# Kernel tuning notes

Measured on AMD Instinct MI355X. Metric: run time of the kernel, lower is better.

The kernel has to match this reference:

```python
import jax, jax.numpy as jnp
import numpy as np

N_NODES = 100000


def leaky(x):
    return jax.nn.leaky_relu(x, negative_slope=0.01)


def gcn_conv(h, W, b, src, dst, n_nodes):
    """PyG GCNConv: add self-loops, symmetric deg^{-1/2} normalization, scatter-add."""
    h = h @ W  # [N, out]
    deg = jax.ops.segment_sum(jnp.ones_like(dst, dtype=h.dtype), dst, num_segments=n_nodes) + 1.0  # +1 self-loop
    dinv = jax.lax.rsqrt(deg)  # deg >= 1 always
    norm = dinv[src] * dinv[dst]  # [E]
    msg = h[src] * norm[:, None]  # gather + scale, [E, out]
    agg = jax.ops.segment_sum(msg, dst, num_segments=n_nodes)
    agg = agg + h * (dinv * dinv)[:, None]  # self-loop message
    return agg + b


def setup_inputs() -> dict:
    key = jax.random.key(0)
    ks = jax.random.split(key, 16)
    num_teams = 100000
    n_edges = 5000000
    n_matches = 1000000
    x = jax.random.randint(ks[0], (N_NODES, 1), 0, num_teams)
    edge_index = jax.random.randint(ks[1], (2, n_edges), 0, N_NODES)
    home = jax.random.randint(ks[2], (n_matches,), 0, N_NODES)
    away = jax.random.randint(ks[3], (n_matches,), 0, N_NODES)
    emb = jax.random.normal(ks[4], (num_teams, 3), dtype=jnp.float32)
    W1 = jax.random.normal(ks[5], (3, 16), dtype=jnp.float32) * (1.0 / np.sqrt(3))
    b1 = jnp.zeros((16,), dtype=jnp.float32)
    W2 = jax.random.normal(ks[6], (16, 3), dtype=jnp.float32) * 0.25
    b2 = jnp.zeros((3,), dtype=jnp.float32)
    lw1 = jax.random.normal(ks[7], (6, 16), dtype=jnp.float32) * (1.0 / np.sqrt(6))
    lb1 = jnp.zeros((16,), dtype=jnp.float32)
    lw2 = jax.random.normal(ks[8], (16, 6), dtype=jnp.float32) * 0.25
    lb2 = jnp.zeros((6,), dtype=jnp.float32)
    lw3 = jax.random.normal(ks[9], (6, 3), dtype=jnp.float32) * (1.0 / np.sqrt(6))
    lb3 = jnp.zeros((3,), dtype=jnp.float32)
    return dict(x=x, edge_index=edge_index, home=home, away=away, emb=emb,
                W1=W1, b1=b1, W2=W2, b2=b2,
                lw1=lw1, lb1=lb1, lw2=lw2, lb2=lb2, lw3=lw3, lb3=lb3)


def reference(x, edge_index, home, away, emb, W1, b1, W2, b2, lw1, lb1, lw2, lb2, lw3, lb3):
    src, dst = edge_index[0], edge_index[1]
    h = emb[x[:, 0]]  # embedding lookup + squeeze(1) -> [N, 3]
    h = leaky(gcn_conv(h, W1, b1, src, dst, N_NODES))  # [N, 16]
    h = leaky(gcn_conv(h, W2, b2, src, dst, N_NODES))  # [N, 3]
    z = jnp.concatenate([h[home], h[away]], axis=-1)  # [M, 6]
    z = leaky(z @ lw1 + lb1)
    z = leaky(z @ lw2 + lb2)
    z = leaky(z @ lw3 + lb3)
    return z.reshape(-1, 3)
```

## Files before the change

### kernel.cpp

```cpp
#include <hip/hip_runtime.h>

typedef unsigned int u32;
typedef unsigned short u16;

static __device__ __forceinline__ float leaky(float v) {
    return v >= 0.0f ? v : 0.01f * v;
}

#define P1_CHUNK 8192
#define NBK 512
#define CAPB 16384
#define ASPLIT 4
#define S1F 8388608.0f
#define S2F 2097152.0f

__global__ __launch_bounds__(256) void k_p1scatterA(
        const int* __restrict__ src, const int* __restrict__ dst,
        int* __restrict__ cur, u32* __restrict__ bkt, int nE) {
    __shared__ int sc[NBK];
    __shared__ int loff[NBK];
    __shared__ int gb[NBK];
    __shared__ int lcur[NBK];
    __shared__ u32 pay[P1_CHUNK];
    __shared__ u16 bb[P1_CHUNK];
    int t = threadIdx.x;
    sc[t] = 0; sc[t + 256] = 0;
    __syncthreads();
    int base = blockIdx.x * P1_CHUNK;
    int lim = min(P1_CHUNK, nE - base);
    if (lim == P1_CHUNK) {
        const int4* p = (const int4*)(dst + base);
        for (int i = t; i < P1_CHUNK / 4; i += 256) {
            int4 v = p[i];
            atomicAdd(&sc[v.x >> 8], 1);
            atomicAdd(&sc[v.y >> 8], 1);
            atomicAdd(&sc[v.z >> 8], 1);
            atomicAdd(&sc[v.w >> 8], 1);
        }
    } else {
        for (int i = t; i < lim; i += 256)
            atomicAdd(&sc[dst[base + i] >> 8], 1);
    }
    __syncthreads();
    int c0 = sc[t], c1 = sc[t + 256];
    gb[t]       = (t << 14)         + ((c0 > 0) ? atomicAdd(&cur[t], c0) : 0);
    gb[t + 256] = ((t + 256) << 14) + ((c1 > 0) ? atomicAdd(&cur[t + 256], c1) : 0);
    for (int o = 1; o < NBK; o <<= 1) {
        __syncthreads();
        int a0 = (t >= o) ? sc[t - o] : 0;
        int a1 = (t + 256 >= o) ? sc[t + 256 - o] : 0;
        __syncthreads();
        sc[t] += a0; sc[t + 256] += a1;
    }
    __syncthreads();
    loff[t] = sc[t] - c0;           loff[t + 256] = sc[t + 256] - c1;
    lcur[t] = loff[t];              lcur[t + 256] = loff[t + 256];
    __syncthreads();
    int n4 = lim >> 2;
    const int4* d4p = (const int4*)(dst + base);
    const int4* s4p = (const int4*)(src + base);
    for (int i = t; i < n4; i += 256) {
        int4 d4 = d4p[i];
        int4 s4 = s4p[i];
        int b, r;
        b = d4.x >> 8; r = atomicAdd(&lcur[b], 1);
        pay[r] = (u32)(((d4.x & 255) << 17) | s4.x); bb[r] = (u16)b;
        b = d4.y >> 8; r = atomicAdd(&lcur[b], 1);
        pay[r] = (u32)(((d4.y & 255) << 17) | s4.y); bb[r] = (u16)b;
        b = d4.z >> 8; r = atomicAdd(&lcur[b], 1);
        pay[r] = (u32)(((d4.z & 255) << 17) | s4.z); bb[r] = (u16)b;
        b = d4.w >> 8; r = atomicAdd(&lcur[b], 1);
        pay[r] = (u32)(((d4.w & 255) << 17) | s4.w); bb[r] = (u16)b;
    }
    for (int i = (n4 << 2) + t; i < lim; i += 256) {
        int d = dst[base + i], s = src[base + i];
        int b = d >> 8;
        int r = atomicAdd(&lcur[b], 1);
        pay[r] = (u32)(((d & 255) << 17) | s);
        bb[r] = (u16)b;
    }
    __syncthreads();
    for (int i = t; i < lim; i += 256) {
        int b = bb[i];
        bkt[gb[b] + (i - loff[b])] = pay[i];
    }
}

__global__ __launch_bounds__(256) void k_cnt1F(
        const u32* __restrict__ bkt, const int* __restrict__ cur,
        const int* __restrict__ x, const float* __restrict__ emb,
        float* __restrict__ dinv, float4* __restrict__ hd0, int nN) {
    __shared__ int h[256];
    int t = threadIdx.x, b = blockIdx.x;
    int base = b << 14;
    int end = base + cur[b];
    h[t] = 0;
    __syncthreads();
    int vend = base + ((end - base) & ~3);
    for (int i = base + t * 4; i < vend; i += 256 * 4) {
        uint4 v = *(const uint4*)&bkt[i];
        atomicAdd(&h[v.x >> 17], 1);
        atomicAdd(&h[v.y >> 17], 1);
        atomicAdd(&h[v.z >> 17], 1);
        atomicAdd(&h[v.w >> 17], 1);
    }
    if (vend + t < end) atomicAdd(&h[bkt[vend + t] >> 17], 1);
    __syncthreads();
    int d = b * 256 + t;
    if (d < nN) {
        float di = rsqrtf((float)h[t] + 1.0f);
        dinv[d] = di;
        int xi = x[d] * 3;
        hd0[d] = make_float4(emb[xi] * di, emb[xi + 1] * di, emb[xi + 2] * di, 0.f);
    }
}

__global__ __launch_bounds__(256) void k_aggIF(
        const u32* __restrict__ bkt, const int* __restrict__ cur,
        const float4* __restrict__ tab, float* __restrict__ pacc,
        float scale, float inv_scale) {
    __shared__ int acc[768];
    int t = threadIdx.x;
    int blk = blockIdx.x, b = blk >> 2, s = blk & 3;
    int base = b << 14;
    int sz = cur[b];
    int chunk = (sz + ASPLIT - 1) / ASPLIT;
    int st = min(base + s * chunk, base + sz);
    int en = min(st + chunk, base + sz);
    acc[t] = 0; acc[t + 256] = 0; acc[t + 512] = 0;
    __syncthreads();
    int a0 = min((st + 3) & ~3, en);
    if (st + t < a0) {
        u32 v = bkt[st + t];
        float4 h = tab[v & 0x1FFFFu];
        int bin = (int)(v >> 17) * 3;
        atomicAdd(&acc[bin + 0], __float2int_rn(h.x * scale));
        atomicAdd(&acc[bin + 1], __float2int_rn(h.y * scale));
        atomicAdd(&acc[bin + 2], __float2int_rn(h.z * scale));
    }
    int vend = a0 + ((en - a0) & ~3);
    for (int i = a0 + t * 4; i < vend; i += 256 * 4) {
        uint4 v = *(const uint4*)&bkt[i];
        float4 h0 = tab[v.x & 0x1FFFFu];
        float4 h1 = tab[v.y & 0x1FFFFu];
        float4 h2 = tab[v.z & 0x1FFFFu];
        float4 h3 = tab[v.w & 0x1FFFFu];
        int b0 = (int)(v.x >> 17) * 3, b1 = (int)(v.y >> 17) * 3;
        int b2 = (int)(v.z >> 17) * 3, b3 = (int)(v.w >> 17) * 3;
        atomicAdd(&acc[b0 + 0], __float2int_rn(h0.x * scale));
        atomicAdd(&acc[b0 + 1], __float2int_rn(h0.y * scale));
        atomicAdd(&acc[b0 + 2], __float2int_rn(h0.z * scale));
        atomicAdd(&acc[b1 + 0], __float2int_rn(h1.x * scale));
        atomicAdd(&acc[b1 + 1], __float2int_rn(h1.y * scale));
        atomicAdd(&acc[b1 + 2], __float2int_rn(h1.z * scale));
        atomicAdd(&acc[b2 + 0], __float2int_rn(h2.x * scale));
        atomicAdd(&acc[b2 + 1], __float2int_rn(h2.y * scale));
        atomicAdd(&acc[b2 + 2], __float2int_rn(h2.z * scale));
        atomicAdd(&acc[b3 + 0], __float2int_rn(h3.x * scale));
        atomicAdd(&acc[b3 + 1], __float2int_rn(h3.y * scale));
        atomicAdd(&acc[b3 + 2], __float2int_rn(h3.z * scale));
    }
    if (vend + t < en) {
        u32 v = bkt[vend + t];
        float4 h = tab[v & 0x1FFFFu];
        int bin = (int)(v >> 17) * 3;
        atomicAdd(&acc[bin + 0], __float2int_rn(h.x * scale));
        atomicAdd(&acc[bin + 1], __float2int_rn(h.y * scale));
        atomicAdd(&acc[bin + 2], __float2int_rn(h.z * scale));
    }
    __syncthreads();
    float* p = pacc + (size_t)blk * 768;
    p[t]       = (float)acc[t * 3 + 0] * inv_scale;
    p[t + 256] = (float)acc[t * 3 + 1] * inv_scale;
    p[t + 512] = (float)acc[t * 3 + 2] * inv_scale;
}

__global__ void k_fin1(const float* __restrict__ pacc, const float* __restrict__ dinv,
                       const float4* __restrict__ hd0,
                       const float* __restrict__ W1, const float* __restrict__ b1,
                       const float* __restrict__ W2,
                       float4* __restrict__ hd2, int nN) {
    int d = blockIdx.x * blockDim.x + threadIdx.x;
    if (d >= nN) return;
    int b = d >> 8, q = d & 255;
    float s0 = 0.f, s1 = 0.f, s2 = 0.f;
#pragma unroll
    for (int s = 0; s < ASPLIT; ++s) {
        const float* p = pacc + (size_t)(b * ASPLIT + s) * 768;
        s0 += p[q]; s1 += p[q + 256]; s2 += p[q + 512];
    }
    float di = dinv[d];
    float4 self = hd0[d];
    float a0 = di * (s0 + self.x);
    float a1 = di * (s1 + self.y);
    float a2 = di * (s2 + self.z);
    float o0 = 0.f, o1 = 0.f, o2 = 0.f;
#pragma unroll
    for (int k = 0; k < 16; ++k) {
        float p = leaky(a0 * W1[k] + a1 * W1[16 + k] + a2 * W1[32 + k] + b1[k]);
        o0 += p * W2[k * 3 + 0];
        o1 += p * W2[k * 3 + 1];
        o2 += p * W2[k * 3 + 2];
    }
    hd2[d] = make_float4(o0 * di, o1 * di, o2 * di, 0.f);
}

__global__ void k_fin2(const float* __restrict__ pacc, const float* __restrict__ dinv,
                       const float4* __restrict__ hd2, const float* __restrict__ b2,
                       float4* __restrict__ h2, int nN) {
    int d = blockIdx.x * blockDim.x + threadIdx.x;
    if (d >= nN) return;
    int b = d >> 8, q = d & 255;
    float s0 = 0.f, s1 = 0.f, s2 = 0.f;
#pragma unroll
    for (int s = 0; s < ASPLIT; ++s) {
        const float* p = pacc + (size_t)(b * ASPLIT + s) * 768;
        s0 += p[q]; s1 += p[q + 256]; s2 += p[q + 512];
    }
    float di = dinv[d];
    float4 self = hd2[d];
    h2[d] = make_float4(leaky(di * (s0 + self.x) + b2[0]),
                        leaky(di * (s1 + self.y) + b2[1]),
                        leaky(di * (s2 + self.z) + b2[2]), 0.f);
}

__global__ __launch_bounds__(256) void k_mlp4v(
        const int* __restrict__ home, const int* __restrict__ away,
        const float4* __restrict__ h2,
        const float* __restrict__ lw1, const float* __restrict__ lb1,
        const float* __restrict__ lw2, const float* __restrict__ lb2,
        const float* __restrict__ lw3, const float* __restrict__ lb3,
        float* __restrict__ out, int nM) {
    __shared__ float s[235];
    int t = threadIdx.x;
    if (t < 96)       s[t] = lw1[t];
    else if (t < 112) s[t] = lb1[t - 96];
    else if (t < 208) s[t] = lw2[t - 112];
    else if (t < 214) s[t] = lb2[t - 208];
    else if (t < 232) s[t] = lw3[t - 214];
    else if (t < 235) s[t] = lb3[t - 232];
    __syncthreads();
    const float* sw1 = s;        const float* sb1 = s + 96;
    const float* sw2 = s + 112;  const float* sb2 = s + 208;
    const float* sw3 = s + 214;  const float* sb3 = s + 232;
    int i = blockIdx.x * blockDim.x + threadIdx.x;
    int m0 = i * 4;
    if (m0 >= nM) return;
    float res[12];
    int nq = min(4, nM - m0);
    int hidx[4], aidx[4];
    if (nq == 4) {
        int4 hv = *(const int4*)&home[m0];
        int4 av = *(const int4*)&away[m0];
        hidx[0] = hv.x; hidx[1] = hv.y; hidx[2] = hv.z; hidx[3] = hv.w;
        aidx[0] = av.x; aidx[1] = av.y; aidx[2] = av.z; aidx[3] = av.w;
    } else {
        for (int j = 0; j < nq; ++j) { hidx[j] = home[m0 + j]; aidx[j] = away[m0 + j]; }
    }
    for (int j = 0; j < nq; ++j) {
        float4 zh = h2[hidx[j]];
        float4 za = h2[aidx[j]];
        float z[6] = {zh.x, zh.y, zh.z, za.x, za.y, za.z};
        float t1[16];
#pragma unroll
        for (int k = 0; k < 16; ++k) {
            float p = sb1[k];
#pragma unroll
            for (int q = 0; q < 6; ++q) p += z[q] * sw1[q * 16 + k];
            t1[k] = leaky(p);
        }
        float t2[6];
#pragma unroll
        for (int k = 0; k < 6; ++k) {
            float p = sb2[k];
#pragma unroll
            for (int q = 0; q < 16; ++q) p += t1[q] * sw2[q * 6 + k];
            t2[k] = leaky(p);
        }
#pragma unroll
        for (int k = 0; k < 3; ++k) {
            float p = sb3[k];
#pragma unroll
            for (int q = 0; q < 6; ++q) p += t2[q] * sw3[q * 3 + k];
            res[j * 3 + k] = leaky(p);
        }
    }
    if (nq == 4) {
        float4* o4 = (float4*)&out[m0 * 3];
        o4[0] = make_float4(res[0], res[1], res[2], res[3]);
        o4[1] = make_float4(res[4], res[5], res[6], res[7]);
        o4[2] = make_float4(res[8], res[9], res[10], res[11]);
    } else {
        for (int j = 0; j < nq * 3; ++j) out[m0 * 3 + j] = res[j];
    }
}

__global__ void f_deg(const int* __restrict__ dst, float* __restrict__ deg, int nE) {
    int e = blockIdx.x * blockDim.x + threadIdx.x;
    if (e < nE) atomicAdd(&deg[dst[e]], 1.0f);
}
__global__ void f_hd0(const int* __restrict__ x, const float* __restrict__ emb,
                      float* __restrict__ dinv, float4* __restrict__ hd0, int nN) {
    int i = blockIdx.x * blockDim.x + threadIdx.x;
    if (i >= nN) return;
    float di = rsqrtf(dinv[i] + 1.0f);
    dinv[i] = di;
    int xi = x[i] * 3;
    hd0[i] = make_float4(emb[xi] * di, emb[xi + 1] * di, emb[xi + 2] * di, 0.f);
}
__global__ void f_scatter(const int* __restrict__ src, const int* __restrict__ dst,
                          const float4* __restrict__ tab, float* __restrict__ agg, int nE) {
    int e = blockIdx.x * blockDim.x + threadIdx.x;
    if (e >= nE) return;
    int s = src[e], d = dst[e];
    float4 v = tab[s];
    atomicAdd(&agg[d * 3 + 0], v.x);
    atomicAdd(&agg[d * 3 + 1], v.y);
    atomicAdd(&agg[d * 3 + 2], v.z);
}
__global__ void f_fin1(const float* __restrict__ agg, const float* __restrict__ dinv,
                       const float4* __restrict__ hd0,
                       const float* __restrict__ W1, const float* __restrict__ b1,
                       const float* __restrict__ W2, float4* __restrict__ hd2, int nN) {
    int d = blockIdx.x * blockDim.x + threadIdx.x;
    if (d >= nN) return;
    float di = dinv[d];
    float4 self = hd0[d];
    float a0 = di * (agg[d * 3 + 0] + self.x);
    float a1 = di * (agg[d * 3 + 1] + self.y);
    float a2 = di * (agg[d * 3 + 2] + self.z);
    float o0 = 0.f, o1 = 0.f, o2 = 0.f;
#pragma unroll
    for (int k = 0; k < 16; ++k) {
        float p = leaky(a0 * W1[k] + a1 * W1[16 + k] + a2 * W1[32 + k] + b1[k]);
        o0 += p * W2[k * 3 + 0];
        o1 += p * W2[k * 3 + 1];
        o2 += p * W2[k * 3 + 2];
    }
    hd2[d] = make_float4(o0 * di, o1 * di, o2 * di, 0.f);
}
__global__ void f_fin2(const float* __restrict__ agg, const float* __restrict__ dinv,
                       const float4* __restrict__ hd2, const float* __restrict__ b2,
                       float4* __restrict__ h2, int nN) {
    int d = blockIdx.x * blockDim.x + threadIdx.x;
    if (d >= nN) return;
    float di = dinv[d];
    float4 self = hd2[d];
    h2[d] = make_float4(leaky(di * (agg[d * 3 + 0] + self.x) + b2[0]),
                        leaky(di * (agg[d * 3 + 1] + self.y) + b2[1]),
                        leaky(di * (agg[d * 3 + 2] + self.z) + b2[2]), 0.f);
}

extern "C" void kernel_launch(void* const* d_in, const int* in_sizes, int n_in,
                              void* d_out, int out_size, void* d_ws, size_t ws_size,
                              hipStream_t stream) {
    const int*   x    = (const int*)d_in[0];
    const int*   ei   = (const int*)d_in[1];
    const int*   home = (const int*)d_in[2];
    const int*   away = (const int*)d_in[3];
    const float* emb  = (const float*)d_in[4];
    const float* W1   = (const float*)d_in[5];
    const float* b1   = (const float*)d_in[6];
    const float* W2   = (const float*)d_in[7];
    const float* b2   = (const float*)d_in[8];
    const float* lw1  = (const float*)d_in[9];
    const float* lb1  = (const float*)d_in[10];
    const float* lw2  = (const float*)d_in[11];
    const float* lb2  = (const float*)d_in[12];
    const float* lw3  = (const float*)d_in[13];
    const float* lb3  = (const float*)d_in[14];
    float* out = (float*)d_out;

    const int nN = in_sizes[0];
    const int nE = in_sizes[1] / 2;
    const int nM = in_sizes[2];
    const int* src = ei;
    const int* dst = ei + nE;
    const int B = 256;

    const int nb1 = (nE + P1_CHUNK - 1) / P1_CHUNK;
    const size_t paccN = (size_t)NBK * ASPLIT * 768;
    const size_t bktN = (size_t)NBK * CAPB;

    size_t need = (size_t)3 * nN * 16 + bktN * 4 + paccN * 4 +
                  (size_t)nN * 4 + NBK * 4;

    double mean_b = (double)nE * 256.0 / (double)nN;
    double sig_b = sqrt(mean_b);
    bool cap_ok = (mean_b + 10.0 * sig_b) < (double)CAPB;

    if (nN <= NBK * 256 && ws_size >= need && cap_ok) {
        char* w = (char*)d_ws;
        float4* hd0 = (float4*)w;                 w += (size_t)nN * 16;
        float4* hd2 = (float4*)w;                 w += (size_t)nN * 16;
        float4* h2  = (float4*)w;                 w += (size_t)nN * 16;
        u32* bkt  = (u32*)w;                      w += bktN * 4;
        float* pacc = (float*)w;                  w += paccN * 4;
        float* dinv = (float*)w;                  w += (size_t)nN * 4;
        int* cur  = (int*)w;

        hipMemsetAsync(cur, 0, NBK * sizeof(int), stream);
        k_p1scatterA<<<nb1, 256, 0, stream>>>(src, dst, cur, bkt, nE);
        k_cnt1F<<<NBK, 256, 0, stream>>>(bkt, cur, x, emb, dinv, hd0, nN);
        k_aggIF<<<NBK * ASPLIT, 256, 0, stream>>>(bkt, cur, hd0, pacc,
                                                  S1F, 1.0f / S1F);
        k_fin1<<<(nN + B - 1) / B, B, 0, stream>>>(pacc, dinv, hd0, W1, b1, W2,
                                                   hd2, nN);
        k_aggIF<<<NBK * ASPLIT, 256, 0, stream>>>(bkt, cur, hd2, pacc,
                                                  S2F, 1.0f / S2F);
        k_fin2<<<(nN + B - 1) / B, B, 0, stream>>>(pacc, dinv, hd2, b2, h2, nN);
        int nQuads = (nM + 3) / 4;
        k_mlp4v<<<(nQuads + B - 1) / B, B, 0, stream>>>(home, away, h2,
                                                        lw1, lb1, lw2, lb2,
                                                        lw3, lb3, out, nM);
    } else {
        char* w = (char*)d_ws;
        float4* hd0 = (float4*)w;                 w += (size_t)nN * 16;
        float4* hd2 = (float4*)w;                 w += (size_t)nN * 16;
        float4* h2  = (float4*)w;                 w += (size_t)nN * 16;
        float* agg  = (float*)w;                  w += (size_t)3 * nN * 4;
        float* dinv = (float*)w;

        hipMemsetAsync(dinv, 0, (size_t)nN * sizeof(float), stream);
        hipMemsetAsync(agg, 0, (size_t)3 * nN * sizeof(float), stream);
        f_deg<<<(nE + B - 1) / B, B, 0, stream>>>(dst, dinv, nE);
        f_hd0<<<(nN + B - 1) / B, B, 0, stream>>>(x, emb, dinv, hd0, nN);
        f_scatter<<<(nE + B - 1) / B, B, 0, stream>>>(src, dst, hd0, agg, nE);
        f_fin1<<<(nN + B - 1) / B, B, 0, stream>>>(agg, dinv, hd0, W1, b1, W2, hd2, nN);
        hipMemsetAsync(agg, 0, (size_t)3 * nN * sizeof(float), stream);
        f_scatter<<<(nE + B - 1) / B, B, 0, stream>>>(src, dst, hd2, agg, nE);
        f_fin2<<<(nN + B - 1) / B, B, 0, stream>>>(agg, dinv, hd2, b2, h2, nN);
        int nQuads = (nM + 3) / 4;
        k_mlp4v<<<(nQuads + B - 1) / B, B, 0, stream>>>(home, away, h2,
                                                        lw1, lb1, lw2, lb2,
                                                        lw3, lb3, out, nM);
    }
}
```

Baseline: 136.2 us.

## Coarsen destination buckets to 2048 nodes with 64 buckets and 16-way split

Edges are now binned into 64 coarse destination buckets of 2048 nodes each instead of 512 buckets of 256 nodes. The scatter kernel uses a wave-level shuffle scan over 64 counters in place of a shared-memory scan over 512, and its chunk shrinks to 4096 edges. The aggregation kernel keeps larger 6144-entry shared accumulators, and each bucket is split 16 ways so enough blocks remain. This is meant to improve write coalescing in the scatter and cut per-bucket overhead. The cost is more LDS per block, which may lower occupancy, plus more partial sums for the finalize kernels to reduce.

New measurement: 176.4 us. +29.5%, slower.

```diff
diff --git a/kernel.cpp b/kernel.cpp
--- a/kernel.cpp
+++ b/kernel.cpp
@@ -1,60 +1,59 @@
 #include <hip/hip_runtime.h>
 
 typedef unsigned int u32;
-typedef unsigned short u16;
+typedef unsigned char u8;
 
 static __device__ __forceinline__ float leaky(float v) {
     return v >= 0.0f ? v : 0.01f * v;
 }
 
-#define P1_CHUNK 8192
-#define NBK 512
-#define CAPB 16384
-#define ASPLIT 4
+#define P1C 4096
+#define NB2 64
+#define CAP2_LOG 17
+#define ASPL2 16
 #define S1F 8388608.0f
 #define S2F 2097152.0f
 
-__global__ __launch_bounds__(256) void k_p1scatterA(
+__global__ __launch_bounds__(256) void k_p1scatterB(
         const int* __restrict__ src, const int* __restrict__ dst,
         int* __restrict__ cur, u32* __restrict__ bkt, int nE) {
-    __shared__ int sc[NBK];
-    __shared__ int loff[NBK];
-    __shared__ int gb[NBK];
-    __shared__ int lcur[NBK];
-    __shared__ u32 pay[P1_CHUNK];
-    __shared__ u16 bb[P1_CHUNK];
+    __shared__ int sc[NB2];
+    __shared__ int loff[NB2];
+    __shared__ int gb[NB2];
+    __shared__ int lcur[NB2];
+    __shared__ u32 pay[P1C];
+    __shared__ u8 bb[P1C];
     int t = threadIdx.x;
-    sc[t] = 0; sc[t + 256] = 0;
-    __syncthreads();
-    int base = blockIdx.x * P1_CHUNK;
-    int lim = min(P1_CHUNK, nE - base);
-    if (lim == P1_CHUNK) {
+    if (t < NB2) sc[t] = 0;
+    __syncthreads();
+    int base = blockIdx.x * P1C;
+    int lim = min(P1C, nE - base);
+    if (lim == P1C) {
         const int4* p = (const int4*)(dst + base);
-        for (int i = t; i < P1_CHUNK / 4; i += 256) {
+        for (int i = t; i < P1C / 4; i += 256) {
             int4 v = p[i];
-            atomicAdd(&sc[v.x >> 8], 1);
-            atomicAdd(&sc[v.y >> 8], 1);
-            atomicAdd(&sc[v.z >> 8], 1);
-            atomicAdd(&sc[v.w >> 8], 1);
+            atomicAdd(&sc[v.x >> 11], 1);
+            atomicAdd(&sc[v.y >> 11], 1);
+            atomicAdd(&sc[v.z >> 11], 1);
+            atomicAdd(&sc[v.w >> 11], 1);
         }
     } else {
         for (int i = t; i < lim; i += 256)
-            atomicAdd(&sc[dst[base + i] >> 8], 1);
-    }
-    __syncthreads();
-    int c0 = sc[t], c1 = sc[t + 256];
-    gb[t]       = (t << 14)         + ((c0 > 0) ? atomicAdd(&cur[t], c0) : 0);
-    gb[t + 256] = ((t + 256) << 14) + ((c1 > 0) ? atomicAdd(&cur[t + 256], c1) : 0);
-    for (int o = 1; o < NBK; o <<= 1) {
-        __syncthreads();
-        int a0 = (t >= o) ? sc[t - o] : 0;
-        int a1 = (t + 256 >= o) ? sc[t + 256 - o] : 0;
-        __syncthreads();
-        sc[t] += a0; sc[t + 256] += a1;
-    }
-    __syncthreads();
-    loff[t] = sc[t] - c0;           loff[t + 256] = sc[t + 256] - c1;
-    lcur[t] = loff[t];              lcur[t + 256] = loff[t + 256];
+            atomicAdd(&sc[dst[base + i] >> 11], 1);
+    }
+    __syncthreads();
+    if (t < NB2) {
+        int c = sc[t];
+        gb[t] = (t << CAP2_LOG) + ((c > 0) ? atomicAdd(&cur[t], c) : 0);
+        int incl = c;
+#pragma unroll
+        for (int o = 1; o < NB2; o <<= 1) {
+            int xv = __shfl_up(incl, o);
+            if (t >= o) incl += xv;
+        }
+        loff[t] = incl - c;
+        lcur[t] = incl - c;
+    }
     __syncthreads();
     int n4 = lim >> 2;
     const int4* d4p = (const int4*)(dst + base);
@@ -63,21 +62,21 @@
         int4 d4 = d4p[i];
         int4 s4 = s4p[i];
         int b, r;
-        b = d4.x >> 8; r = atomicAdd(&lcur[b], 1);
-        pay[r] = (u32)(((d4.x & 255) << 17) | s4.x); bb[r] = (u16)b;
-        b = d4.y >> 8; r = atomicAdd(&lcur[b], 1);
-        pay[r] = (u32)(((d4.y & 255) << 17) | s4.y); bb[r] = (u16)b;
-        b = d4.z >> 8; r = atomicAdd(&lcur[b], 1);
-        pay[r] = (u32)(((d4.z & 255) << 17) | s4.z); bb[r] = (u16)b;
-        b = d4.w >> 8; r = atomicAdd(&lcur[b], 1);
-        pay[r] = (u32)(((d4.w & 255) << 17) | s4.w); bb[r] = (u16)b;
+        b = d4.x >> 11; r = atomicAdd(&lcur[b], 1);
+        pay[r] = (u32)(((d4.x & 2047) << 17) | s4.x); bb[r] = (u8)b;
+        b = d4.y >> 11; r = atomicAdd(&lcur[b], 1);
+        pay[r] = (u32)(((d4.y & 2047) << 17) | s4.y); bb[r] = (u8)b;
+        b = d4.z >> 11; r = atomicAdd(&lcur[b], 1);
+        pay[r] = (u32)(((d4.z & 2047) << 17) | s4.z); bb[r] = (u8)b;
+        b = d4.w >> 11; r = atomicAdd(&lcur[b], 1);
+        pay[r] = (u32)(((d4.w & 2047) << 17) | s4.w); bb[r] = (u8)b;
     }
     for (int i = (n4 << 2) + t; i < lim; i += 256) {
         int d = dst[base + i], s = src[base + i];
-        int b = d >> 8;
+        int b = d >> 11;
         int r = atomicAdd(&lcur[b], 1);
-        pay[r] = (u32)(((d & 255) << 17) | s);
-        bb[r] = (u16)b;
+        pay[r] = (u32)(((d & 2047) << 17) | s);
+        bb[r] = (u8)b;
     }
     __syncthreads();
     for (int i = t; i < lim; i += 256) {
@@ -86,18 +85,18 @@
     }
 }
 
-__global__ __launch_bounds__(256) void k_cnt1F(
+__global__ __launch_bounds__(256) void k_cntB(
         const u32* __restrict__ bkt, const int* __restrict__ cur,
         const int* __restrict__ x, const float* __restrict__ emb,
         float* __restrict__ dinv, float4* __restrict__ hd0, int nN) {
-    __shared__ int h[256];
+    __shared__ int h[2048];
     int t = threadIdx.x, b = blockIdx.x;
-    int base = b << 14;
+    for (int k = t; k < 2048; k += 256) h[k] = 0;
+    __syncthreads();
+    int base = b << CAP2_LOG;
     int end = base + cur[b];
-    h[t] = 0;
-    __syncthreads();
     int vend = base + ((end - base) & ~3);
-    for (int i = base + t * 4; i < vend; i += 256 * 4) {
+    for (int i = base + t * 4; i < vend; i += 1024) {
         uint4 v = *(const uint4*)&bkt[i];
         atomicAdd(&h[v.x >> 17], 1);
         atomicAdd(&h[v.y >> 17], 1);
@@ -106,28 +105,33 @@
     }
     if (vend + t < end) atomicAdd(&h[bkt[vend + t] >> 17], 1);
     __syncthreads();
-    int d = b * 256 + t;
-    if (d < nN) {
-        float di = rsqrtf((float)h[t] + 1.0f);
-        dinv[d] = di;
-        int xi = x[d] * 3;
-        hd0[d] = make_float4(emb[xi] * di, emb[xi + 1] * di, emb[xi + 2] * di, 0.f);
-    }
-}
-
-__global__ __launch_bounds__(256) void k_aggIF(
+#pragma unroll
+    for (int k = 0; k < 8; ++k) {
+        int bin = t + k * 256;
+        int d = b * 2048 + bin;
+        if (d < nN) {
+            float di = rsqrtf((float)h[bin] + 1.0f);
+            dinv[d] = di;
+            int xi = x[d] * 3;
+            hd0[d] = make_float4(emb[xi] * di, emb[xi + 1] * di,
+                                 emb[xi + 2] * di, 0.f);
+        }
+    }
+}
+
+__global__ __launch_bounds__(256) void k_aggB(
         const u32* __restrict__ bkt, const int* __restrict__ cur,
         const float4* __restrict__ tab, float* __restrict__ pacc,
         float scale, float inv_scale) {
-    __shared__ int acc[768];
+    __shared__ int acc[6144];
     int t = threadIdx.x;
-    int blk = blockIdx.x, b = blk >> 2, s = blk & 3;
-    int base = b << 14;
+    int blk = blockIdx.x, b = blk >> 4, s = blk & 15;
+    int base = b << CAP2_LOG;
     int sz = cur[b];
-    int chunk = (sz + ASPLIT - 1) / ASPLIT;
+    int chunk = (sz + ASPL2 - 1) / ASPL2;
     int st = min(base + s * chunk, base + sz);
     int en = min(st + chunk, base + sz);
-    acc[t] = 0; acc[t + 256] = 0; acc[t + 512] = 0;
+    for (int k = t; k < 6144; k += 256) acc[k] = 0;
     __syncthreads();
     int a0 = min((st + 3) & ~3, en);
     if (st + t < a0) {
@@ -139,7 +143,7 @@
         atomicAdd(&acc[bin + 2], __float2int_rn(h.z * scale));
     }
     int vend = a0 + ((en - a0) & ~3);
-    for (int i = a0 + t * 4; i < vend; i += 256 * 4) {
+    for (int i = a0 + t * 4; i < vend; i += 1024) {
         uint4 v = *(const uint4*)&bkt[i];
         float4 h0 = tab[v.x & 0x1FFFFu];
         float4 h1 = tab[v.y & 0x1FFFFu];
@@ -169,25 +173,30 @@
         atomicAdd(&acc[bin + 2], __float2int_rn(h.z * scale));
     }
     __syncthreads();
-    float* p = pacc + (size_t)blk * 768;
-    p[t]       = (float)acc[t * 3 + 0] * inv_scale;
-    p[t + 256] = (float)acc[t * 3 + 1] * inv_scale;
-    p[t + 512] = (float)acc[t * 3 + 2] * inv_scale;
-}
-
-__global__ void k_fin1(const float* __restrict__ pacc, const float* __restrict__ dinv,
-                       const float4* __restrict__ hd0,
-                       const float* __restrict__ W1, const float* __restrict__ b1,
-                       const float* __restrict__ W2,
-                       float4* __restrict__ hd2, int nN) {
+    float* p = pacc + (size_t)blk * 6144;
+#pragma unroll
+    for (int k = 0; k < 8; ++k) {
+        int bin = t + k * 256;
+        p[bin]        = (float)acc[bin * 3 + 0] * inv_scale;
+        p[bin + 2048] = (float)acc[bin * 3 + 1] * inv_scale;
+        p[bin + 4096] = (float)acc[bin * 3 + 2] * inv_scale;
+    }
+}
+
+__global__ void k_fin1B(const float* __restrict__ pacc, const float* __restrict__ dinv,
+                        const float4* __restrict__ hd0,
+                        const float* __restrict__ W1, const float* __restrict__ b1,
+                        const float* __restrict__ W2,
+                        float4* __restrict__ hd2, int nN) {
     int d = blockIdx.x * blockDim.x + threadIdx.x;
     if (d >= nN) return;
-    int b = d >> 8, q = d & 255;
+    int b = d >> 11, q = d & 2047;
+    const float* pb = pacc + (size_t)b * ASPL2 * 6144;
     float s0 = 0.f, s1 = 0.f, s2 = 0.f;
 #pragma unroll
-    for (int s = 0; s < ASPLIT; ++s) {
-        const float* p = pacc + (size_t)(b * ASPLIT + s) * 768;
-        s0 += p[q]; s1 += p[q + 256]; s2 += p[q + 512];
+    for (int s = 0; s < ASPL2; ++s) {
+        const float* p = pb + s * 6144;
+        s0 += p[q]; s1 += p[q + 2048]; s2 += p[q + 4096];
     }
     float di = dinv[d];
     float4 self = hd0[d];
@@ -205,17 +214,18 @@
     hd2[d] = make_float4(o0 * di, o1 * di, o2 * di, 0.f);
 }
 
-__global__ void k_fin2(const float* __restrict__ pacc, const float* __restrict__ dinv,
-                       const float4* __restrict__ hd2, const float* __restrict__ b2,
-                       float4* __restrict__ h2, int nN) {
+__global__ void k_fin2B(const float* __restrict__ pacc, const float* __restrict__ dinv,
+                        const float4* __restrict__ hd2, const float* __restrict__ b2,
+                        float4* __restrict__ h2, int nN) {
     int d = blockIdx.x * blockDim.x + threadIdx.x;
     if (d >= nN) return;
-    int b = d >> 8, q = d & 255;
+    int b = d >> 11, q = d & 2047;
+    const float* pb = pacc + (size_t)b * ASPL2 * 6144;
     float s0 = 0.f, s1 = 0.f, s2 = 0.f;
 #pragma unroll
-    for (int s = 0; s < ASPLIT; ++s) {
-        const float* p = pacc + (size_t)(b * ASPLIT + s) * 768;
-        s0 += p[q]; s1 += p[q + 256]; s2 += p[q + 512];
+    for (int s = 0; s < ASPL2; ++s) {
+        const float* p = pb + s * 6144;
+        s0 += p[q]; s1 += p[q + 2048]; s2 += p[q + 4096];
     }
     float di = dinv[d];
     float4 self = hd2[d];
@@ -378,18 +388,19 @@
     const int* dst = ei + nE;
     const int B = 256;
 
-    const int nb1 = (nE + P1_CHUNK - 1) / P1_CHUNK;
-    const size_t paccN = (size_t)NBK * ASPLIT * 768;
-    const size_t bktN = (size_t)NBK * CAPB;
+    const int nb1 = (nE + P1C - 1) / P1C;
+    const int nB2 = (nN + 2047) / 2048;
+    const size_t bktN = (size_t)nB2 << CAP2_LOG;
+    const size_t paccN = (size_t)nB2 * ASPL2 * 6144;
 
     size_t need = (size_t)3 * nN * 16 + bktN * 4 + paccN * 4 +
-                  (size_t)nN * 4 + NBK * 4;
-
-    double mean_b = (double)nE * 256.0 / (double)nN;
+                  (size_t)nN * 4 + NB2 * 4;
+
+    double mean_b = (double)nE * 2048.0 / (double)nN;
     double sig_b = sqrt(mean_b);
-    bool cap_ok = (mean_b + 10.0 * sig_b) < (double)CAPB;
-
-    if (nN <= NBK * 256 && ws_size >= need && cap_ok) {
+    bool cap_ok = (mean_b + 10.0 * sig_b) < (double)(1 << CAP2_LOG);
+
+    if (nN <= NB2 * 2048 && ws_size >= need && cap_ok) {
         char* w = (char*)d_ws;
         float4* hd0 = (float4*)w;                 w += (size_t)nN * 16;
         float4* hd2 = (float4*)w;                 w += (size_t)nN * 16;
@@ -399,16 +410,16 @@
         float* dinv = (float*)w;                  w += (size_t)nN * 4;
         int* cur  = (int*)w;
 
-        hipMemsetAsync(cur, 0, NBK * sizeof(int), stream);
-        k_p1scatterA<<<nb1, 256, 0, stream>>>(src, dst, cur, bkt, nE);
-        k_cnt1F<<<NBK, 256, 0, stream>>>(bkt, cur, x, emb, dinv, hd0, nN);
-        k_aggIF<<<NBK * ASPLIT, 256, 0, stream>>>(bkt, cur, hd0, pacc,
-                                                  S1F, 1.0f / S1F);
-        k_fin1<<<(nN + B - 1) / B, B, 0, stream>>>(pacc, dinv, hd0, W1, b1, W2,
-                                                   hd2, nN);
-        k_aggIF<<<NBK * ASPLIT, 256, 0, stream>>>(bkt, cur, hd2, pacc,
-                                                  S2F, 1.0f / S2F);
-        k_fin2<<<(nN + B - 1) / B, B, 0, stream>>>(pacc, dinv, hd2, b2, h2, nN);
+        hipMemsetAsync(cur, 0, NB2 * sizeof(int), stream);
+        k_p1scatterB<<<nb1, 256, 0, stream>>>(src, dst, cur, bkt, nE);
+        k_cntB<<<nB2, 256, 0, stream>>>(bkt, cur, x, emb, dinv, hd0, nN);
+        k_aggB<<<nB2 * ASPL2, 256, 0, stream>>>(bkt, cur, hd0, pacc,
+                                                S1F, 1.0f / S1F);
+        k_fin1B<<<(nN + B - 1) / B, B, 0, stream>>>(pacc, dinv, hd0, W1, b1, W2,
+                                                    hd2, nN);
+        k_aggB<<<nB2 * ASPL2, 256, 0, stream>>>(bkt, cur, hd2, pacc,
+                                                S2F, 1.0f / S2F);
+        k_fin2B<<<(nN + B - 1) / B, B, 0, stream>>>(pacc, dinv, hd2, b2, h2, nN);
         int nQuads = (nM + 3) / 4;
         k_mlp4v<<<(nQuads + B - 1) / B, B, 0, stream>>>(home, away, h2,
                                                         lw1, lb1, lw2, lb2,
```

## Widen scatter and count blocks, use wave-shuffle scan, split aggregation eightfold

Applied to the files above, without the earlier changes.

The bucket scatter kernel moves from 256 to 512 threads and replaces its shared-memory Hillis-Steele prefix scan with a 64-lane shuffle scan plus a per-wave carry. The degree-count kernel runs 1024 threads per bucket, and aggregation splits each bucket into 8 sub-blocks instead of 4. The aim is more parallelism per bucket and fewer barriers. The cost is more partial-accumulator traffic in aggregation, and the pacc buffer size must match the larger split.

Measured after the change: 130.6 us. 4.1% less time.

```diff
diff --git a/kernel.cpp b/kernel.cpp
--- a/kernel.cpp
+++ b/kernel.cpp
@@ -8,29 +8,31 @@
 }
 
 #define P1_CHUNK 8192
+#define P1T 512
 #define NBK 512
 #define CAPB 16384
-#define ASPLIT 4
+#define ASPLIT 8
 #define S1F 8388608.0f
 #define S2F 2097152.0f
 
-__global__ __launch_bounds__(256) void k_p1scatterA(
+__global__ __launch_bounds__(512) void k_p1scatterA(
         const int* __restrict__ src, const int* __restrict__ dst,
         int* __restrict__ cur, u32* __restrict__ bkt, int nE) {
     __shared__ int sc[NBK];
     __shared__ int loff[NBK];
     __shared__ int gb[NBK];
     __shared__ int lcur[NBK];
+    __shared__ int wsum[8];
     __shared__ u32 pay[P1_CHUNK];
     __shared__ u16 bb[P1_CHUNK];
     int t = threadIdx.x;
-    sc[t] = 0; sc[t + 256] = 0;
+    sc[t] = 0;
     __syncthreads();
     int base = blockIdx.x * P1_CHUNK;
     int lim = min(P1_CHUNK, nE - base);
     if (lim == P1_CHUNK) {
         const int4* p = (const int4*)(dst + base);
-        for (int i = t; i < P1_CHUNK / 4; i += 256) {
+        for (int i = t; i < P1_CHUNK / 4; i += P1T) {
             int4 v = p[i];
             atomicAdd(&sc[v.x >> 8], 1);
             atomicAdd(&sc[v.y >> 8], 1);
@@ -38,28 +40,37 @@
             atomicAdd(&sc[v.w >> 8], 1);
         }
     } else {
-        for (int i = t; i < lim; i += 256)
+        for (int i = t; i < lim; i += P1T)
             atomicAdd(&sc[dst[base + i] >> 8], 1);
     }
     __syncthreads();
-    int c0 = sc[t], c1 = sc[t + 256];
-    gb[t]       = (t << 14)         + ((c0 > 0) ? atomicAdd(&cur[t], c0) : 0);
-    gb[t + 256] = ((t + 256) << 14) + ((c1 > 0) ? atomicAdd(&cur[t + 256], c1) : 0);
-    for (int o = 1; o < NBK; o <<= 1) {
-        __syncthreads();
-        int a0 = (t >= o) ? sc[t - o] : 0;
-        int a1 = (t + 256 >= o) ? sc[t + 256 - o] : 0;
-        __syncthreads();
-        sc[t] += a0; sc[t + 256] += a1;
-    }
-    __syncthreads();
-    loff[t] = sc[t] - c0;           loff[t + 256] = sc[t + 256] - c1;
-    lcur[t] = loff[t];              lcur[t + 256] = loff[t + 256];
+    int c = sc[t];
+    int lane = t & 63;
+    int incl = c;
+#pragma unroll
+    for (int o = 1; o < 64; o <<= 1) {
+        int xv = __shfl_up(incl, o);
+        if (lane >= o) incl += xv;
+    }
+    if (lane == 63) wsum[t >> 6] = incl;
+    __syncthreads();
+    if (t == 0) {
+        int run = 0;
+#pragma unroll
+        for (int k = 0; k < 8; ++k) { int v = wsum[k]; wsum[k] = run; run += v; }
+    }
+    __syncthreads();
+    {
+        int excl = incl - c + wsum[t >> 6];
+        loff[t] = excl;
+        lcur[t] = excl;
+        gb[t] = (t << 14) + ((c > 0) ? atomicAdd(&cur[t], c) : 0);
+    }
     __syncthreads();
     int n4 = lim >> 2;
     const int4* d4p = (const int4*)(dst + base);
     const int4* s4p = (const int4*)(src + base);
-    for (int i = t; i < n4; i += 256) {
+    for (int i = t; i < n4; i += P1T) {
         int4 d4 = d4p[i];
         int4 s4 = s4p[i];
         int b, r;
@@ -72,7 +83,7 @@
         b = d4.w >> 8; r = atomicAdd(&lcur[b], 1);
         pay[r] = (u32)(((d4.w & 255) << 17) | s4.w); bb[r] = (u16)b;
     }
-    for (int i = (n4 << 2) + t; i < lim; i += 256) {
+    for (int i = (n4 << 2) + t; i < lim; i += P1T) {
         int d = dst[base + i], s = src[base + i];
         int b = d >> 8;
         int r = atomicAdd(&lcur[b], 1);
@@ -80,24 +91,24 @@
         bb[r] = (u16)b;
     }
     __syncthreads();
-    for (int i = t; i < lim; i += 256) {
+    for (int i = t; i < lim; i += P1T) {
         int b = bb[i];
         bkt[gb[b] + (i - loff[b])] = pay[i];
     }
 }
 
-__global__ __launch_bounds__(256) void k_cnt1F(
+__global__ __launch_bounds__(1024) void k_cnt1F(
         const u32* __restrict__ bkt, const int* __restrict__ cur,
         const int* __restrict__ x, const float* __restrict__ emb,
         float* __restrict__ dinv, float4* __restrict__ hd0, int nN) {
     __shared__ int h[256];
     int t = threadIdx.x, b = blockIdx.x;
+    if (t < 256) h[t] = 0;
+    __syncthreads();
     int base = b << 14;
     int end = base + cur[b];
-    h[t] = 0;
-    __syncthreads();
     int vend = base + ((end - base) & ~3);
-    for (int i = base + t * 4; i < vend; i += 256 * 4) {
+    for (int i = base + t * 4; i < vend; i += 1024 * 4) {
         uint4 v = *(const uint4*)&bkt[i];
         atomicAdd(&h[v.x >> 17], 1);
         atomicAdd(&h[v.y >> 17], 1);
@@ -106,12 +117,15 @@
     }
     if (vend + t < end) atomicAdd(&h[bkt[vend + t] >> 17], 1);
     __syncthreads();
-    int d = b * 256 + t;
-    if (d < nN) {
-        float di = rsqrtf((float)h[t] + 1.0f);
-        dinv[d] = di;
-        int xi = x[d] * 3;
-        hd0[d] = make_float4(emb[xi] * di, emb[xi + 1] * di, emb[xi + 2] * di, 0.f);
+    if (t < 256) {
+        int d = b * 256 + t;
+        if (d < nN) {
+            float di = rsqrtf((float)h[t] + 1.0f);
+            dinv[d] = di;
+            int xi = x[d] * 3;
+            hd0[d] = make_float4(emb[xi] * di, emb[xi + 1] * di,
+                                 emb[xi + 2] * di, 0.f);
+        }
     }
 }
 
@@ -121,7 +135,7 @@
         float scale, float inv_scale) {
     __shared__ int acc[768];
     int t = threadIdx.x;
-    int blk = blockIdx.x, b = blk >> 2, s = blk & 3;
+    int blk = blockIdx.x, b = blk >> 3, s = blk & 7;
     int base = b << 14;
     int sz = cur[b];
     int chunk = (sz + ASPLIT - 1) / ASPLIT;
@@ -400,8 +414,8 @@
         int* cur  = (int*)w;
 
         hipMemsetAsync(cur, 0, NBK * sizeof(int), stream);
-        k_p1scatterA<<<nb1, 256, 0, stream>>>(src, dst, cur, bkt, nE);
-        k_cnt1F<<<NBK, 256, 0, stream>>>(bkt, cur, x, emb, dinv, hd0, nN);
+        k_p1scatterA<<<nb1, P1T, 0, stream>>>(src, dst, cur, bkt, nE);
+        k_cnt1F<<<NBK, 1024, 0, stream>>>(bkt, cur, x, emb, dinv, hd0, nN);
         k_aggIF<<<NBK * ASPLIT, 256, 0, stream>>>(bkt, cur, hd0, pacc,
                                                   S1F, 1.0f / S1F);
         k_fin1<<<(nN + B - 1) / B, B, 0, stream>>>(pacc, dinv, hd0, W1, b1, W2,
```
